# Performance work log

Measured on AMD Instinct MI355X. Metric: run time of the kernel, lower is better.

Reference implementation:

```python
import jax, jax.numpy as jnp
import numpy as np
import math

B, S, D, H = 2, 2048, 1024, 16
DK = D // H
THETA = 10000.0

def _rope_tables(seq_len, dk, theta):
    freqs = 1.0 / theta ** (np.arange(0, dk, 2)[: dk // 2].astype(np.float32) / dk)
    t = np.arange(seq_len, dtype=np.float32)
    ang = np.outer(t, freqs)  # [S, dk/2]
    return jnp.asarray(np.cos(ang)), jnp.asarray(np.sin(ang))

def setup_inputs() -> dict:
    key = jax.random.key(0)
    ks = jax.random.split(key, 12)
    init = lambda k, shape: (0.02 * jax.random.normal(k, shape)).astype(jnp.float32)
    cos, sin = _rope_tables(S, DK, THETA)
    mask = jnp.tril(jnp.ones((S, S), dtype=jnp.int32))[None, None]  # [1,1,S,S] causal
    return {
        'Q': jax.random.normal(ks[0], (B, S, D), jnp.float32),
        'K': jax.random.normal(ks[1], (B, S, D), jnp.float32),
        'V': jax.random.normal(ks[2], (B, S, D), jnp.float32),
        'mask': mask,
        'Wq_w': init(ks[3], (D, D)), 'Wq_b': init(ks[4], (D,)),
        'Wk_w': init(ks[5], (D, D)), 'Wk_b': init(ks[6], (D,)),
        'Wv_w': init(ks[7], (D, D)), 'Wv_b': init(ks[8], (D,)),
        'Wo_w': init(ks[9], (D, D)), 'Wo_b': init(ks[10], (D,)),
        'cos': cos, 'sin': sin,
    }

def _apply_rope(x, cos, sin):
    # x: [B, S, H, DK]; cos/sin: [S, DK/2]
    x1 = x[..., 0::2]
    x2 = x[..., 1::2]
    c = cos[None, :, None, :]
    s = sin[None, :, None, :]
    out_even = x1 * c - x2 * s
    out_odd = x1 * s + x2 * c
    return jnp.stack([out_even, out_odd], axis=-1).reshape(x.shape)

def reference(Q, K, V, mask, Wq_w, Wq_b, Wk_w, Wk_b, Wv_w, Wv_b, Wo_w, Wo_b, cos, sin):
    b, s, d = Q.shape
    q = (Q @ Wq_w.T + Wq_b).reshape(b, s, H, DK)
    k = (K @ Wk_w.T + Wk_b).reshape(b, s, H, DK)
    v = (V @ Wv_w.T + Wv_b).reshape(b, s, H, DK)
    q = _apply_rope(q, cos[:s], sin[:s])
    k = _apply_rope(k, cos[:s], sin[:s])
    # [B,H,S,DK]
    q = q.transpose(0, 2, 1, 3)
    k = k.transpose(0, 2, 1, 3)
    v = v.transpose(0, 2, 1, 3)
    scores = jnp.einsum('bhqd,bhkd->bhqk', q, k) / math.sqrt(DK)
    scores = jnp.where(mask == 0, jnp.float32(-1e9), scores)
    probs = jax.nn.softmax(scores, axis=-1)
    out = jnp.einsum('bhqk,bhkd->bhqd', probs, v)  # [B,H,S,DK]
    out = out.transpose(0, 2, 1, 3).reshape(b, s, d)
    return out @ Wo_w.T + Wo_b
```

## Files before the change

kernel.cpp:

```cpp
#include <hip/hip_runtime.h>
#include <cstdint>
#include <cstddef>


typedef __bf16 bf16x8 __attribute__((ext_vector_type(8)));
typedef float floatx4 __attribute__((ext_vector_type(4)));

#define DI __device__ __forceinline__

DI unsigned short f2bf(float f) {
  union { float f; unsigned int u; } v; v.f = f;
  unsigned int r = v.u + 0x7fffu + ((v.u >> 16) & 1u);
  return (unsigned short)(r >> 16);
}

DI unsigned short bfb(float f) {
  __bf16 h = (__bf16)f;
  union { __bf16 h; unsigned short u; } c; c.h = h;
  return c.u;
}

__global__ void cvt_all(const float* __restrict__ Q, const float* __restrict__ K,
                        const float* __restrict__ V, const float* __restrict__ Wq,
                        const float* __restrict__ Wk, const float* __restrict__ Wv,
                        const float* __restrict__ Wo, unsigned short* __restrict__ dst) {
  int i = blockIdx.x * blockDim.x + threadIdx.x;
  const float* s;
  int off;
  if (i < 3145728) {
    if (i < 1048576) { s = Q; off = i; }
    else if (i < 2097152) { s = K; off = i - 1048576; }
    else { s = V; off = i - 2097152; }
  } else {
    int j = i - 3145728;
    int wsel = j >> 18;
    off = j & 262143;
    s = (wsel == 0) ? Wq : (wsel == 1) ? Wk : (wsel == 2) ? Wv : Wo;
  }
  float4 f = reinterpret_cast<const float4*>(s)[off];
  ushort4 o;
  o.x = f2bf(f.x); o.y = f2bf(f.y); o.z = f2bf(f.z); o.w = f2bf(f.w);
  reinterpret_cast<ushort4*>(dst)[i] = o;
}

__global__ __launch_bounds__(256)
void gemm_qkv(const unsigned short* __restrict__ Qb, const unsigned short* __restrict__ Kb,
              const unsigned short* __restrict__ Vb, const unsigned short* __restrict__ Wq,
              const unsigned short* __restrict__ Wk, const unsigned short* __restrict__ Wv,
              const float* __restrict__ bq, const float* __restrict__ bk,
              const float* __restrict__ bv, unsigned short* __restrict__ qh,
              unsigned short* __restrict__ kh, unsigned short* __restrict__ vtp,
              const float* __restrict__ cosT, const float* __restrict__ sinT) {
  __shared__ unsigned short As[2][128 * 32];
  __shared__ unsigned short Bs[2][128 * 32];

  const int id = blockIdx.x;
  const int xb = id / 96;
  const int rem = id - xb * 96;
  const int proj = rem >> 5;
  const int yb = rem & 31;

  const unsigned short* X = (proj == 0) ? Qb : (proj == 1) ? Kb : Vb;
  const unsigned short* W = (proj == 0) ? Wq : (proj == 1) ? Wk : Wv;
  const float* bias = (proj == 0) ? bq : (proj == 1) ? bk : bv;
  unsigned short* outB = (proj == 0) ? qh : (proj == 1) ? kh : vtp;

  const int t = threadIdx.x;
  const int lane = t & 63;
  const int w = t >> 6;
  const int row0 = yb * 128;
  const int col0 = xb * 128;
  const int wm = (w >> 1) * 64;
  const int wn = (w & 1) * 64;
  const int fr = lane & 15;
  const int fk = (lane >> 4) * 8;
  const int rbase = (lane >> 4) * 4;

  const int c0 = t, c1 = t + 256;
  const unsigned short* gA0 = X + (size_t)(row0 + (c0 >> 2)) * 1024 + (c0 & 3) * 8;
  const unsigned short* gA1 = X + (size_t)(row0 + (c1 >> 2)) * 1024 + (c1 & 3) * 8;
  const unsigned short* gB0 = W + (size_t)(col0 + (c0 >> 2)) * 1024 + (c0 & 3) * 8;
  const unsigned short* gB1 = W + (size_t)(col0 + (c1 >> 2)) * 1024 + (c1 & 3) * 8;

  floatx4 acc[4][4];
#pragma unroll
  for (int i = 0; i < 4; ++i)
#pragma unroll
    for (int j = 0; j < 4; ++j)
      acc[i][j] = (floatx4){0.f, 0.f, 0.f, 0.f};

  uint4 ra0, ra1, rb0, rb1;
  auto gload = [&](int k0) {
    ra0 = *reinterpret_cast<const uint4*>(gA0 + k0);
    ra1 = *reinterpret_cast<const uint4*>(gA1 + k0);
    rb0 = *reinterpret_cast<const uint4*>(gB0 + k0);
    rb1 = *reinterpret_cast<const uint4*>(gB1 + k0);
  };
  auto swrite = [&](int buf) {
    *reinterpret_cast<uint4*>(&As[buf][c0 * 8]) = ra0;
    *reinterpret_cast<uint4*>(&As[buf][c1 * 8]) = ra1;
    *reinterpret_cast<uint4*>(&Bs[buf][c0 * 8]) = rb0;
    *reinterpret_cast<uint4*>(&Bs[buf][c1 * 8]) = rb1;
  };

  gload(0);
  swrite(0);
  __syncthreads();

  for (int kb = 0; kb < 32; ++kb) {
    const int cur = kb & 1;
    if (kb + 1 < 32) gload((kb + 1) * 32);

    bf16x8 af[4], bfr[4];
#pragma unroll
    for (int i = 0; i < 4; ++i)
      af[i] = *reinterpret_cast<const bf16x8*>(&As[cur][(wm + i * 16 + fr) * 32 + fk]);
#pragma unroll
    for (int j = 0; j < 4; ++j)
      bfr[j] = *reinterpret_cast<const bf16x8*>(&Bs[cur][(wn + j * 16 + fr) * 32 + fk]);
    if (proj == 2) {
#pragma unroll
      for (int i = 0; i < 4; ++i)
#pragma unroll
        for (int j = 0; j < 4; ++j)
          acc[i][j] = __builtin_amdgcn_mfma_f32_16x16x32_bf16(bfr[j], af[i], acc[i][j], 0, 0, 0);
    } else {
#pragma unroll
      for (int i = 0; i < 4; ++i)
#pragma unroll
        for (int j = 0; j < 4; ++j)
          acc[i][j] = __builtin_amdgcn_mfma_f32_16x16x32_bf16(af[i], bfr[j], acc[i][j], 0, 0, 0);
    }

    if (kb + 1 < 32) swrite(cur ^ 1);
    __syncthreads();
  }

  if (proj < 2) {
#pragma unroll
    for (int j = 0; j < 4; ++j) {
      const int col = col0 + wn + j * 16 + fr;
      const float bvv = bias[col];
#pragma unroll
      for (int i = 0; i < 4; ++i) {
#pragma unroll
        for (int r = 0; r < 4; ++r) {
          const int row = row0 + wm + i * 16 + rbase + r;
          float v = acc[i][j][r] + bvv;
          const int bb = row >> 11, sp = row & 2047, hh = col >> 6, dk = col & 63;
          float p = __shfl_xor(v, 1);
          const int i2 = (col & 63) >> 1;
          const float cv = cosT[sp * 32 + i2];
          const float sv = sinT[sp * 32 + i2];
          float res = ((col & 1) == 0) ? (v * cv - p * sv) : (p * sv + v * cv);
          if (proj == 0) res *= 0.125f;
          outB[(((size_t)(bb * 16 + hh)) * 2048 + sp) * 64 + dk] = f2bf(res);
        }
      }
    }
  } else {
#pragma unroll
    for (int j = 0; j < 4; ++j) {
#pragma unroll
      for (int r = 0; r < 4; ++r) {
        const int dkc = col0 + wn + j * 16 + rbase + r;
        const float bvv = bias[dkc];
        const int hh = dkc >> 6, dk = dkc & 63;
#pragma unroll
        for (int i = 0; i < 4; ++i) {
          const int spf = row0 + wm + i * 16 + fr;
          const int bb = spf >> 11, sp = spf & 2047;
          vtp[(((size_t)(bb * 16 + hh)) * 64 + dk) * 2048 + sp] = f2bf(acc[i][j][r] + bvv);
        }
      }
    }
  }
}

__global__ __launch_bounds__(256)
void gemm_out(const unsigned short* __restrict__ X, const unsigned short* __restrict__ W,
              const float* __restrict__ bias, float* __restrict__ outF) {
  __shared__ unsigned short As[2][64 * 32];
  __shared__ unsigned short Bs[2][128 * 32];

  const int id = blockIdx.x;
  const int xb = id >> 6;
  const int yb = id & 63;

  const int t = threadIdx.x;
  const int lane = t & 63;
  const int w = t >> 6;
  const int row0 = yb * 64;
  const int col0 = xb * 128;
  const int wm = (w >> 1) * 32;
  const int wn = (w & 1) * 64;
  const int fr = lane & 15;
  const int fk = (lane >> 4) * 8;
  const int rbase = (lane >> 4) * 4;

  const int c0 = t, c1 = t + 256;
  const unsigned short* gA0 = X + (size_t)(row0 + (c0 >> 2)) * 1024 + (c0 & 3) * 8;
  const unsigned short* gB0 = W + (size_t)(col0 + (c0 >> 2)) * 1024 + (c0 & 3) * 8;
  const unsigned short* gB1 = W + (size_t)(col0 + (c1 >> 2)) * 1024 + (c1 & 3) * 8;

  floatx4 acc[2][4];
#pragma unroll
  for (int i = 0; i < 2; ++i)
#pragma unroll
    for (int j = 0; j < 4; ++j)
      acc[i][j] = (floatx4){0.f, 0.f, 0.f, 0.f};

  uint4 ra0, rb0, rb1;
  auto gload = [&](int k0) {
    ra0 = *reinterpret_cast<const uint4*>(gA0 + k0);
    rb0 = *reinterpret_cast<const uint4*>(gB0 + k0);
    rb1 = *reinterpret_cast<const uint4*>(gB1 + k0);
  };
  auto swrite = [&](int buf) {
    *reinterpret_cast<uint4*>(&As[buf][c0 * 8]) = ra0;
    *reinterpret_cast<uint4*>(&Bs[buf][c0 * 8]) = rb0;
    *reinterpret_cast<uint4*>(&Bs[buf][c1 * 8]) = rb1;
  };

  gload(0);
  swrite(0);
  __syncthreads();

  for (int kb = 0; kb < 32; ++kb) {
    const int cur = kb & 1;
    if (kb + 1 < 32) gload((kb + 1) * 32);

    bf16x8 af[2], bfr[4];
#pragma unroll
    for (int i = 0; i < 2; ++i)
      af[i] = *reinterpret_cast<const bf16x8*>(&As[cur][(wm + i * 16 + fr) * 32 + fk]);
#pragma unroll
    for (int j = 0; j < 4; ++j)
      bfr[j] = *reinterpret_cast<const bf16x8*>(&Bs[cur][(wn + j * 16 + fr) * 32 + fk]);
#pragma unroll
    for (int i = 0; i < 2; ++i)
#pragma unroll
      for (int j = 0; j < 4; ++j)
        acc[i][j] = __builtin_amdgcn_mfma_f32_16x16x32_bf16(af[i], bfr[j], acc[i][j], 0, 0, 0);

    if (kb + 1 < 32) swrite(cur ^ 1);
    __syncthreads();
  }

#pragma unroll
  for (int j = 0; j < 4; ++j) {
    const int col = col0 + wn + j * 16 + fr;
    const float bvv = bias[col];
#pragma unroll
    for (int i = 0; i < 2; ++i)
#pragma unroll
      for (int r = 0; r < 4; ++r) {
        const int row = row0 + wm + i * 16 + rbase + r;
        outF[(size_t)row * 1024 + col] = acc[i][j][r] + bvv;
      }
  }
}

__global__ __launch_bounds__(256)
void flash_attn(const unsigned short* __restrict__ qh,
                const unsigned short* __restrict__ kh,
                const unsigned short* __restrict__ vt,
                unsigned short* __restrict__ out) {
  __shared__ unsigned short Ks[2][64 * 64];
  __shared__ unsigned short Vs[2][64 * 64];
  __shared__ unsigned short Ps[8][16 * 64];

  const int t = threadIdx.x, lane = t & 63, w = t >> 6;
  const int g = lane >> 4;
  const int fr = lane & 15;
  const int fk = g * 8;
  const int rbase = g * 4;
  const int id = blockIdx.x;
  const int qbA = id >> 5;
  const int bh = id & 31;
  const int qbB = 31 - qbA;
  const int qwA = qbA * 64 + w * 16;
  const int qwB = qbB * 64 + w * 16;

  const size_t baseQK = (size_t)bh * 2048 * 64;
  const size_t baseV = (size_t)bh * 64 * 2048;

  bf16x8 qfA[2], qfB[2];
  qfA[0] = *reinterpret_cast<const bf16x8*>(&qh[baseQK + (size_t)(qwA + fr) * 64 + fk]);
  qfA[1] = *reinterpret_cast<const bf16x8*>(&qh[baseQK + (size_t)(qwA + fr) * 64 + 32 + fk]);
  qfB[0] = *reinterpret_cast<const bf16x8*>(&qh[baseQK + (size_t)(qwB + fr) * 64 + fk]);
  qfB[1] = *reinterpret_cast<const bf16x8*>(&qh[baseQK + (size_t)(qwB + fr) * 64 + 32 + fk]);

  floatx4 oA[4], oB[4];
  float lA[4], lB[4];
#pragma unroll
  for (int i = 0; i < 4; ++i) {
    oA[i] = (floatx4){0.f, 0.f, 0.f, 0.f};
    oB[i] = (floatx4){0.f, 0.f, 0.f, 0.f};
    lA[i] = 0.f; lB[i] = 0.f;
  }

  const int sc0 = t, sc1 = t + 256;
  const int r0 = sc0 >> 3, cc0 = sc0 & 7, d0 = (r0 * 8 + (cc0 ^ (r0 & 7))) * 8;
  const int r1 = sc1 >> 3, cc1 = sc1 & 7, d1 = (r1 * 8 + (cc1 ^ (r1 & 7))) * 8;

  uint4 rk0, rk1, rv0, rv1;
  auto gload = [&](int kb) {
    const int k0 = kb * 64;
    rk0 = *reinterpret_cast<const uint4*>(kh + baseQK + (size_t)(k0 + r0) * 64 + cc0 * 8);
    rk1 = *reinterpret_cast<const uint4*>(kh + baseQK + (size_t)(k0 + r1) * 64 + cc1 * 8);
    rv0 = *reinterpret_cast<const uint4*>(vt + baseV + (size_t)r0 * 2048 + k0 + cc0 * 8);
    rv1 = *reinterpret_cast<const uint4*>(vt + baseV + (size_t)r1 * 2048 + k0 + cc1 * 8);
  };
  auto swrite = [&](int buf) {
    *reinterpret_cast<uint4*>(&Ks[buf][d0]) = rk0;
    *reinterpret_cast<uint4*>(&Ks[buf][d1]) = rk1;
    *reinterpret_cast<uint4*>(&Vs[buf][d0]) = rv0;
    *reinterpret_cast<uint4*>(&Vs[buf][d1]) = rv1;
  };

  const int nkb = qbB + 1;
  gload(0);
  swrite(0);
  __syncthreads();

  for (int kb = 0; kb < nkb; ++kb) {
    const int cur = kb & 1;
    if (kb + 1 < nkb) gload(kb + 1);
    const int k0 = kb * 64;
    const bool aAct = (kb <= qbA);

    bf16x8 kf[4][2];
#pragma unroll
    for (int j = 0; j < 4; ++j)
#pragma unroll
      for (int kk = 0; kk < 2; ++kk)
        kf[j][kk] = *reinterpret_cast<const bf16x8*>(
            &Ks[cur][(j * 16 + fr) * 64 + ((((kk << 2) | g) ^ (fr & 7)) << 3)]);

    floatx4 sB[4], sA[4];
#pragma unroll
    for (int j = 0; j < 4; ++j) {
      sB[j] = (floatx4){0.f, 0.f, 0.f, 0.f};
      sA[j] = (floatx4){0.f, 0.f, 0.f, 0.f};
    }
#pragma unroll
    for (int j = 0; j < 4; ++j)
#pragma unroll
      for (int kk = 0; kk < 2; ++kk)
        sB[j] = __builtin_amdgcn_mfma_f32_16x16x32_bf16(qfB[kk], kf[j][kk], sB[j], 0, 0, 0);
    if (aAct) {
#pragma unroll
      for (int j = 0; j < 4; ++j)
#pragma unroll
        for (int kk = 0; kk < 2; ++kk)
          sA[j] = __builtin_amdgcn_mfma_f32_16x16x32_bf16(qfA[kk], kf[j][kk], sA[j], 0, 0, 0);
    }

    if (k0 + 63 > qwB) {
#pragma unroll
      for (int j = 0; j < 4; ++j)
#pragma unroll
        for (int r = 0; r < 4; ++r)
          if (k0 + j * 16 + fr > qwB + rbase + r) sB[j][r] = -1e30f;
    }
    if (aAct && k0 + 63 > qwA) {
#pragma unroll
      for (int j = 0; j < 4; ++j)
#pragma unroll
        for (int r = 0; r < 4; ++r)
          if (k0 + j * 16 + fr > qwA + rbase + r) sA[j][r] = -1e30f;
    }

#pragma unroll
    for (int j = 0; j < 4; ++j) {
      const int chb = (j * 16 + fr) >> 3;
      const int cin = fr & 7;
#pragma unroll
      for (int r = 0; r < 4; ++r) {
        const int row = rbase + r;
        float pB = __expf(sB[j][r]);
        lB[r] += pB;
        Ps[w][row * 64 + ((chb ^ (row & 7)) << 3) + cin] = bfb(pB);
      }
    }
    if (aAct) {
#pragma unroll
      for (int j = 0; j < 4; ++j) {
        const int chb = (j * 16 + fr) >> 3;
        const int cin = fr & 7;
#pragma unroll
        for (int r = 0; r < 4; ++r) {
          const int row = rbase + r;
          float pA = __expf(sA[j][r]);
          lA[r] += pA;
          Ps[w + 4][row * 64 + ((chb ^ (row & 7)) << 3) + cin] = bfb(pA);
        }
      }
    }

    bf16x8 vf[4][2], pB2[2], pA2[2];
#pragma unroll
    for (int id2 = 0; id2 < 4; ++id2)
#pragma unroll
      for (int kk = 0; kk < 2; ++kk)
        vf[id2][kk] = *reinterpret_cast<const bf16x8*>(
            &Vs[cur][(id2 * 16 + fr) * 64 + ((((kk << 2) | g) ^ (fr & 7)) << 3)]);
#pragma unroll
    for (int kk = 0; kk < 2; ++kk)
      pB2[kk] = *reinterpret_cast<const bf16x8*>(
          &Ps[w][fr * 64 + ((((kk << 2) | g) ^ (fr & 7)) << 3)]);
#pragma unroll
    for (int kk = 0; kk < 2; ++kk)
#pragma unroll
      for (int id2 = 0; id2 < 4; ++id2)
        oB[id2] = __builtin_amdgcn_mfma_f32_16x16x32_bf16(pB2[kk], vf[id2][kk], oB[id2], 0, 0, 0);
    if (aAct) {
#pragma unroll
      for (int kk = 0; kk < 2; ++kk)
        pA2[kk] = *reinterpret_cast<const bf16x8*>(
            &Ps[w + 4][fr * 64 + ((((kk << 2) | g) ^ (fr & 7)) << 3)]);
#pragma unroll
      for (int kk = 0; kk < 2; ++kk)
#pragma unroll
        for (int id2 = 0; id2 < 4; ++id2)
          oA[id2] = __builtin_amdgcn_mfma_f32_16x16x32_bf16(pA2[kk], vf[id2][kk], oA[id2], 0, 0, 0);
    }

    if (kb + 1 < nkb) swrite(cur ^ 1);
    __syncthreads();
  }

#pragma unroll
  for (int r = 0; r < 4; ++r) {
#pragma unroll
    for (int d = 1; d < 16; d <<= 1) {
      lB[r] += __shfl_xor(lB[r], d);
      lA[r] += __shfl_xor(lA[r], d);
    }
  }

  const int bb = bh >> 4, hh = bh & 15;
#pragma unroll
  for (int id2 = 0; id2 < 4; ++id2)
#pragma unroll
    for (int r = 0; r < 4; ++r) {
      const int qrA = qwA + rbase + r;
      const int qrB = qwB + rbase + r;
      out[((size_t)(bb * 2048 + qrA)) * 1024 + hh * 64 + id2 * 16 + fr] = bfb(oA[id2][r] / lA[r]);
      out[((size_t)(bb * 2048 + qrB)) * 1024 + hh * 64 + id2 * 16 + fr] = bfb(oB[id2][r] / lB[r]);
    }
}

extern "C" void kernel_launch(void* const* d_in, const int* in_sizes, int n_in,
                              void* d_out, int out_size, void* d_ws, size_t ws_size,
                              hipStream_t stream) {
  const float* Q  = (const float*)d_in[0];
  const float* K  = (const float*)d_in[1];
  const float* V  = (const float*)d_in[2];
  const float* Wq = (const float*)d_in[4];
  const float* bq = (const float*)d_in[5];
  const float* Wk = (const float*)d_in[6];
  const float* bk = (const float*)d_in[7];
  const float* Wv = (const float*)d_in[8];
  const float* bv = (const float*)d_in[9];
  const float* Wo = (const float*)d_in[10];
  const float* bo = (const float*)d_in[11];
  const float* cosT = (const float*)d_in[12];
  const float* sinT = (const float*)d_in[13];

  char* ws = (char*)d_ws;
  const size_t MB = 1024 * 1024;
  unsigned short* Qb  = (unsigned short*)(ws + 0 * MB);
  unsigned short* Kb  = (unsigned short*)(ws + 8 * MB);
  unsigned short* Vb  = (unsigned short*)(ws + 16 * MB);
  unsigned short* Wqb = (unsigned short*)(ws + 24 * MB);
  unsigned short* Wkb = (unsigned short*)(ws + 26 * MB);
  unsigned short* Wvb = (unsigned short*)(ws + 28 * MB);
  unsigned short* Wob = (unsigned short*)(ws + 30 * MB);
  unsigned short* qh  = (unsigned short*)(ws + 32 * MB);
  unsigned short* khp = (unsigned short*)(ws + 40 * MB);
  unsigned short* vtp = (unsigned short*)(ws + 48 * MB);
  unsigned short* ao  = (unsigned short*)(ws + 56 * MB);

  cvt_all<<<16384, 256, 0, stream>>>(Q, K, V, Wq, Wk, Wv, Wo, (unsigned short*)ws);

  gemm_qkv<<<768, 256, 0, stream>>>(Qb, Kb, Vb, Wqb, Wkb, Wvb, bq, bk, bv,
                                    qh, khp, vtp, cosT, sinT);
  flash_attn<<<512, 256, 0, stream>>>(qh, khp, vtp, ao);
  gemm_out<<<512, 256, 0, stream>>>(ao, Wob, bo, (float*)d_out);
}
```

Before: 248.4 us.

## Use direct global-to-LDS loads with triple-buffered pipeline in GEMMs and attention

```diff
diff --git a/kernel.cpp b/kernel.cpp
--- a/kernel.cpp
+++ b/kernel.cpp
@@ -18,6 +18,12 @@
   __bf16 h = (__bf16)f;
   union { __bf16 h; unsigned short u; } c; c.h = h;
   return c.u;
+}
+
+DI void gld16(const void* g, void* l) {
+  __builtin_amdgcn_global_load_lds(
+      (const __attribute__((address_space(1))) void*)g,
+      (__attribute__((address_space(3))) void*)l, 16, 0, 0);
 }
 
 __global__ void cvt_all(const float* __restrict__ Q, const float* __restrict__ K,
@@ -51,8 +57,8 @@
               const float* __restrict__ bv, unsigned short* __restrict__ qh,
               unsigned short* __restrict__ kh, unsigned short* __restrict__ vtp,
               const float* __restrict__ cosT, const float* __restrict__ sinT) {
-  __shared__ unsigned short As[2][128 * 32];
-  __shared__ unsigned short Bs[2][128 * 32];
+  __shared__ unsigned short As[3][128 * 32];
+  __shared__ unsigned short Bs[3][128 * 32];
 
   const int id = blockIdx.x;
   const int xb = id / 96;
@@ -89,27 +95,23 @@
     for (int j = 0; j < 4; ++j)
       acc[i][j] = (floatx4){0.f, 0.f, 0.f, 0.f};
 
-  uint4 ra0, ra1, rb0, rb1;
-  auto gload = [&](int k0) {
-    ra0 = *reinterpret_cast<const uint4*>(gA0 + k0);
-    ra1 = *reinterpret_cast<const uint4*>(gA1 + k0);
-    rb0 = *reinterpret_cast<const uint4*>(gB0 + k0);
-    rb1 = *reinterpret_cast<const uint4*>(gB1 + k0);
+  auto stage = [&](int buf, int k0) {
+    gld16(gA0 + k0, &As[buf][c0 * 8]);
+    gld16(gA1 + k0, &As[buf][c1 * 8]);
+    gld16(gB0 + k0, &Bs[buf][c0 * 8]);
+    gld16(gB1 + k0, &Bs[buf][c1 * 8]);
   };
-  auto swrite = [&](int buf) {
-    *reinterpret_cast<uint4*>(&As[buf][c0 * 8]) = ra0;
-    *reinterpret_cast<uint4*>(&As[buf][c1 * 8]) = ra1;
-    *reinterpret_cast<uint4*>(&Bs[buf][c0 * 8]) = rb0;
-    *reinterpret_cast<uint4*>(&Bs[buf][c1 * 8]) = rb1;
-  };
-
-  gload(0);
-  swrite(0);
-  __syncthreads();
-
+
+  stage(0, 0);
+  stage(1, 32);
+  asm volatile("s_waitcnt vmcnt(4)" ::: "memory");
+  __builtin_amdgcn_s_barrier();
+  __builtin_amdgcn_sched_barrier(0);
+
+  int cur = 0;
   for (int kb = 0; kb < 32; ++kb) {
-    const int cur = kb & 1;
-    if (kb + 1 < 32) gload((kb + 1) * 32);
+    const int sb = (cur == 0) ? 2 : cur - 1;
+    if (kb + 2 < 32) stage(sb, (kb + 2) * 32);
 
     bf16x8 af[4], bfr[4];
 #pragma unroll
@@ -132,8 +134,13 @@
           acc[i][j] = __builtin_amdgcn_mfma_f32_16x16x32_bf16(af[i], bfr[j], acc[i][j], 0, 0, 0);
     }
 
-    if (kb + 1 < 32) swrite(cur ^ 1);
-    __syncthreads();
+    if (kb + 1 < 32) {
+      if (kb + 2 < 32) asm volatile("s_waitcnt vmcnt(4)" ::: "memory");
+      else             asm volatile("s_waitcnt vmcnt(0)" ::: "memory");
+      __builtin_amdgcn_s_barrier();
+      __builtin_amdgcn_sched_barrier(0);
+    }
+    cur = (cur == 2) ? 0 : cur + 1;
   }
 
   if (proj < 2) {
@@ -180,8 +187,8 @@
 __global__ __launch_bounds__(256)
 void gemm_out(const unsigned short* __restrict__ X, const unsigned short* __restrict__ W,
               const float* __restrict__ bias, float* __restrict__ outF) {
-  __shared__ unsigned short As[2][64 * 32];
-  __shared__ unsigned short Bs[2][128 * 32];
+  __shared__ unsigned short As[3][64 * 32];
+  __shared__ unsigned short Bs[3][128 * 32];
 
   const int id = blockIdx.x;
   const int xb = id >> 6;
@@ -210,25 +217,22 @@
     for (int j = 0; j < 4; ++j)
       acc[i][j] = (floatx4){0.f, 0.f, 0.f, 0.f};
 
-  uint4 ra0, rb0, rb1;
-  auto gload = [&](int k0) {
-    ra0 = *reinterpret_cast<const uint4*>(gA0 + k0);
-    rb0 = *reinterpret_cast<const uint4*>(gB0 + k0);
-    rb1 = *reinterpret_cast<const uint4*>(gB1 + k0);
+  auto stage = [&](int buf, int k0) {
+    gld16(gA0 + k0, &As[buf][c0 * 8]);
+    gld16(gB0 + k0, &Bs[buf][c0 * 8]);
+    gld16(gB1 + k0, &Bs[buf][c1 * 8]);
   };
-  auto swrite = [&](int buf) {
-    *reinterpret_cast<uint4*>(&As[buf][c0 * 8]) = ra0;
-    *reinterpret_cast<uint4*>(&Bs[buf][c0 * 8]) = rb0;
-    *reinterpret_cast<uint4*>(&Bs[buf][c1 * 8]) = rb1;
-  };
-
-  gload(0);
-  swrite(0);
-  __syncthreads();
-
+
+  stage(0, 0);
+  stage(1, 32);
+  asm volatile("s_waitcnt vmcnt(3)" ::: "memory");
+  __builtin_amdgcn_s_barrier();
+  __builtin_amdgcn_sched_barrier(0);
+
+  int cur = 0;
   for (int kb = 0; kb < 32; ++kb) {
-    const int cur = kb & 1;
-    if (kb + 1 < 32) gload((kb + 1) * 32);
+    const int sb = (cur == 0) ? 2 : cur - 1;
+    if (kb + 2 < 32) stage(sb, (kb + 2) * 32);
 
     bf16x8 af[2], bfr[4];
 #pragma unroll
@@ -243,8 +247,13 @@
       for (int j = 0; j < 4; ++j)
         acc[i][j] = __builtin_amdgcn_mfma_f32_16x16x32_bf16(af[i], bfr[j], acc[i][j], 0, 0, 0);
 
-    if (kb + 1 < 32) swrite(cur ^ 1);
-    __syncthreads();
+    if (kb + 1 < 32) {
+      if (kb + 2 < 32) asm volatile("s_waitcnt vmcnt(3)" ::: "memory");
+      else             asm volatile("s_waitcnt vmcnt(0)" ::: "memory");
+      __builtin_amdgcn_s_barrier();
+      __builtin_amdgcn_sched_barrier(0);
+    }
+    cur = (cur == 2) ? 0 : cur + 1;
   }
 
 #pragma unroll
@@ -266,8 +275,8 @@
                 const unsigned short* __restrict__ kh,
                 const unsigned short* __restrict__ vt,
                 unsigned short* __restrict__ out) {
-  __shared__ unsigned short Ks[2][64 * 64];
-  __shared__ unsigned short Vs[2][64 * 64];
+  __shared__ unsigned short Ks[3][64 * 64];
+  __shared__ unsigned short Vs[3][64 * 64];
   __shared__ unsigned short Ps[8][16 * 64];
 
   const int t = threadIdx.x, lane = t & 63, w = t >> 6;
@@ -301,32 +310,28 @@
   }
 
   const int sc0 = t, sc1 = t + 256;
-  const int r0 = sc0 >> 3, cc0 = sc0 & 7, d0 = (r0 * 8 + (cc0 ^ (r0 & 7))) * 8;
-  const int r1 = sc1 >> 3, cc1 = sc1 & 7, d1 = (r1 * 8 + (cc1 ^ (r1 & 7))) * 8;
-
-  uint4 rk0, rk1, rv0, rv1;
-  auto gload = [&](int kb) {
+  const int r0 = sc0 >> 3, s0 = (sc0 & 7) ^ (r0 & 7);
+  const int r1 = sc1 >> 3, s1 = (sc1 & 7) ^ (r1 & 7);
+
+  auto stage = [&](int buf, int kb) {
     const int k0 = kb * 64;
-    rk0 = *reinterpret_cast<const uint4*>(kh + baseQK + (size_t)(k0 + r0) * 64 + cc0 * 8);
-    rk1 = *reinterpret_cast<const uint4*>(kh + baseQK + (size_t)(k0 + r1) * 64 + cc1 * 8);
-    rv0 = *reinterpret_cast<const uint4*>(vt + baseV + (size_t)r0 * 2048 + k0 + cc0 * 8);
-    rv1 = *reinterpret_cast<const uint4*>(vt + baseV + (size_t)r1 * 2048 + k0 + cc1 * 8);
+    gld16(kh + baseQK + (size_t)(k0 + r0) * 64 + s0 * 8, &Ks[buf][sc0 * 8]);
+    gld16(kh + baseQK + (size_t)(k0 + r1) * 64 + s1 * 8, &Ks[buf][sc1 * 8]);
+    gld16(vt + baseV + (size_t)r0 * 2048 + k0 + s0 * 8, &Vs[buf][sc0 * 8]);
+    gld16(vt + baseV + (size_t)r1 * 2048 + k0 + s1 * 8, &Vs[buf][sc1 * 8]);
   };
-  auto swrite = [&](int buf) {
-    *reinterpret_cast<uint4*>(&Ks[buf][d0]) = rk0;
-    *reinterpret_cast<uint4*>(&Ks[buf][d1]) = rk1;
-    *reinterpret_cast<uint4*>(&Vs[buf][d0]) = rv0;
-    *reinterpret_cast<uint4*>(&Vs[buf][d1]) = rv1;
-  };
 
   const int nkb = qbB + 1;
-  gload(0);
-  swrite(0);
-  __syncthreads();
-
+  stage(0, 0);
+  stage(1, 1);
+  asm volatile("s_waitcnt vmcnt(4)" ::: "memory");
+  __builtin_amdgcn_s_barrier();
+  __builtin_amdgcn_sched_barrier(0);
+
+  int cur = 0;
   for (int kb = 0; kb < nkb; ++kb) {
-    const int cur = kb & 1;
-    if (kb + 1 < nkb) gload(kb + 1);
+    const int sb = (cur == 0) ? 2 : cur - 1;
+    if (kb + 2 < nkb) stage(sb, kb + 2);
     const int k0 = kb * 64;
     const bool aAct = (kb <= qbA);
 
@@ -427,8 +432,13 @@
           oA[id2] = __builtin_amdgcn_mfma_f32_16x16x32_bf16(pA2[kk], vf[id2][kk], oA[id2], 0, 0, 0);
     }
 
-    if (kb + 1 < nkb) swrite(cur ^ 1);
-    __syncthreads();
+    if (kb + 1 < nkb) {
+      if (kb + 2 < nkb) asm volatile("s_waitcnt vmcnt(4)" ::: "memory");
+      else              asm volatile("s_waitcnt vmcnt(0)" ::: "memory");
+      __builtin_amdgcn_s_barrier();
+      __builtin_amdgcn_sched_barrier(0);
+    }
+    cur = (cur == 2) ? 0 : cur + 1;
   }
 
 #pragma unroll
```

Result: slower. 261.1 us (+5.1%).

## Load K/V MFMA fragments directly from global memory, dropping LDS staging

Applied to the files above, without the earlier changes.

```diff
diff --git a/kernel.cpp b/kernel.cpp
--- a/kernel.cpp
+++ b/kernel.cpp
@@ -266,8 +266,6 @@
                 const unsigned short* __restrict__ kh,
                 const unsigned short* __restrict__ vt,
                 unsigned short* __restrict__ out) {
-  __shared__ unsigned short Ks[2][64 * 64];
-  __shared__ unsigned short Vs[2][64 * 64];
   __shared__ unsigned short Ps[8][16 * 64];
 
   const int t = threadIdx.x, lane = t & 63, w = t >> 6;
@@ -291,6 +289,9 @@
   qfB[0] = *reinterpret_cast<const bf16x8*>(&qh[baseQK + (size_t)(qwB + fr) * 64 + fk]);
   qfB[1] = *reinterpret_cast<const bf16x8*>(&qh[baseQK + (size_t)(qwB + fr) * 64 + 32 + fk]);
 
+  const unsigned short* kP = kh + baseQK + (size_t)fr * 64;
+  const unsigned short* vP = vt + baseV + (size_t)fr * 2048;
+
   floatx4 oA[4], oB[4];
   float lA[4], lB[4];
 #pragma unroll
@@ -300,43 +301,27 @@
     lA[i] = 0.f; lB[i] = 0.f;
   }
 
-  const int sc0 = t, sc1 = t + 256;
-  const int r0 = sc0 >> 3, cc0 = sc0 & 7, d0 = (r0 * 8 + (cc0 ^ (r0 & 7))) * 8;
-  const int r1 = sc1 >> 3, cc1 = sc1 & 7, d1 = (r1 * 8 + (cc1 ^ (r1 & 7))) * 8;
-
-  uint4 rk0, rk1, rv0, rv1;
-  auto gload = [&](int kb) {
-    const int k0 = kb * 64;
-    rk0 = *reinterpret_cast<const uint4*>(kh + baseQK + (size_t)(k0 + r0) * 64 + cc0 * 8);
-    rk1 = *reinterpret_cast<const uint4*>(kh + baseQK + (size_t)(k0 + r1) * 64 + cc1 * 8);
-    rv0 = *reinterpret_cast<const uint4*>(vt + baseV + (size_t)r0 * 2048 + k0 + cc0 * 8);
-    rv1 = *reinterpret_cast<const uint4*>(vt + baseV + (size_t)r1 * 2048 + k0 + cc1 * 8);
-  };
-  auto swrite = [&](int buf) {
-    *reinterpret_cast<uint4*>(&Ks[buf][d0]) = rk0;
-    *reinterpret_cast<uint4*>(&Ks[buf][d1]) = rk1;
-    *reinterpret_cast<uint4*>(&Vs[buf][d0]) = rv0;
-    *reinterpret_cast<uint4*>(&Vs[buf][d1]) = rv1;
-  };
-
   const int nkb = qbB + 1;
-  gload(0);
-  swrite(0);
-  __syncthreads();
 
   for (int kb = 0; kb < nkb; ++kb) {
-    const int cur = kb & 1;
-    if (kb + 1 < nkb) gload(kb + 1);
     const int k0 = kb * 64;
     const bool aAct = (kb <= qbA);
 
+    bf16x8 vf[4][2];
+#pragma unroll
+    for (int id2 = 0; id2 < 4; ++id2)
+#pragma unroll
+      for (int kk = 0; kk < 2; ++kk)
+        vf[id2][kk] = *reinterpret_cast<const bf16x8*>(
+            &vP[(size_t)(id2 * 16) * 2048 + k0 + kk * 32 + fk]);
+
     bf16x8 kf[4][2];
 #pragma unroll
     for (int j = 0; j < 4; ++j)
 #pragma unroll
       for (int kk = 0; kk < 2; ++kk)
         kf[j][kk] = *reinterpret_cast<const bf16x8*>(
-            &Ks[cur][(j * 16 + fr) * 64 + ((((kk << 2) | g) ^ (fr & 7)) << 3)]);
+            &kP[(size_t)(k0 + j * 16) * 64 + kk * 32 + fk]);
 
     floatx4 sB[4], sA[4];
 #pragma unroll
@@ -399,13 +384,7 @@
       }
     }
 
-    bf16x8 vf[4][2], pB2[2], pA2[2];
-#pragma unroll
-    for (int id2 = 0; id2 < 4; ++id2)
-#pragma unroll
-      for (int kk = 0; kk < 2; ++kk)
-        vf[id2][kk] = *reinterpret_cast<const bf16x8*>(
-            &Vs[cur][(id2 * 16 + fr) * 64 + ((((kk << 2) | g) ^ (fr & 7)) << 3)]);
+    bf16x8 pB2[2], pA2[2];
 #pragma unroll
     for (int kk = 0; kk < 2; ++kk)
       pB2[kk] = *reinterpret_cast<const bf16x8*>(
@@ -426,9 +405,6 @@
         for (int id2 = 0; id2 < 4; ++id2)
           oA[id2] = __builtin_amdgcn_mfma_f32_16x16x32_bf16(pA2[kk], vf[id2][kk], oA[id2], 0, 0, 0);
     }
-
-    if (kb + 1 < nkb) swrite(cur ^ 1);
-    __syncthreads();
   }
 
 #pragma unroll
```

Measured after the change: 305.6 us. 23.0% more time.
